# Kernel optimization log

Measured on AMD Instinct MI355X. Metric: run time of the kernel, lower is better.

Reference implementation:

```python
import jax, jax.numpy as jnp
import numpy as np

K = 3        # deform conv kernel size
STRIDE = 1
PAD = 1
DIL = 1


def setup_inputs() -> dict:
    key = jax.random.key(0)
    k1, k2, k3, k4 = jax.random.split(key, 4)
    B, C, H, W, O = 4, 256, 96, 96, 256
    x = jax.random.normal(k1, (B, C, H, W), jnp.float32)
    # offset-predicting conv: 3x3, stride 1, pad 1 -> 2*K*K channels
    # (source inits these to zero; use small random weights so offsets are
    # nonzero but sub-pixel scale, exercising the bilinear-sampling path)
    w_off = jax.random.normal(k2, (2 * K * K, C, 3, 3), jnp.float32) * 0.01
    b_off = jnp.zeros((2 * K * K,), jnp.float32)
    w_dc = jax.random.normal(k3, (O, C, K, K), jnp.float32) * (1.0 / np.sqrt(C * K * K))
    b_dc = jax.random.normal(k4, (O,), jnp.float32) * 0.01
    return {"x": x, "w_off": w_off, "b_off": b_off, "w_dc": w_dc, "b_dc": b_dc}


def _conv2d(x, w, b, stride, pad):
    out = jax.lax.conv_general_dilated(
        x, w, window_strides=(stride, stride),
        padding=[(pad, pad), (pad, pad)],
        dimension_numbers=("NCHW", "OIHW", "NCHW"))
    return out + b[None, :, None, None]


def _deform_conv(x, offset, w_dc, b_dc):
    # x: [B,C,H,W]; offset: [B, 2*K*K, Ho, Wo]; w_dc: [O,C,K,K]
    B, C, H, W = x.shape
    O = w_dc.shape[0]
    Ho = (H + 2 * PAD - DIL * (K - 1) - 1) // STRIDE + 1
    Wo = (W + 2 * PAD - DIL * (K - 1) - 1) // STRIDE + 1
    # mmcv layout: channel = (i*K + j)*2 + {0: dy, 1: dx}
    off = offset.reshape(B, K * K, 2, Ho, Wo)
    iy = jnp.repeat(jnp.arange(K), K)   # kernel row index per tap  [K*K]
    jx = jnp.tile(jnp.arange(K), K)     # kernel col index per tap  [K*K]
    base_y = (jnp.arange(Ho) * STRIDE - PAD)[None, :, None] + (iy * DIL)[:, None, None]  # [K2,Ho,1]
    base_x = (jnp.arange(Wo) * STRIDE - PAD)[None, None, :] + (jx * DIL)[:, None, None]  # [K2,1,Wo]
    py = base_y[None].astype(x.dtype) + off[:, :, 0]  # [B,K2,Ho,Wo]
    px = base_x[None].astype(x.dtype) + off[:, :, 1]  # [B,K2,Ho,Wo]

    y0 = jnp.floor(py)
    x0 = jnp.floor(px)
    ly = py - y0
    lx = px - x0
    y0i = y0.astype(jnp.int32)
    x0i = x0.astype(jnp.int32)

    flat = x.reshape(B, C, H * W)

    def corner(yi, xi, wgt):
        # zero-padding bilinear: out-of-range corners contribute 0
        valid = ((yi >= 0) & (yi < H) & (xi >= 0) & (xi < W)).astype(x.dtype)
        idx = jnp.clip(yi, 0, H - 1) * W + jnp.clip(xi, 0, W - 1)  # [B,K2,Ho,Wo]
        g = jnp.take_along_axis(flat, idx.reshape(B, 1, -1), axis=2)
        g = g.reshape(B, C, K * K, Ho, Wo)
        return g * (wgt * valid)[:, None]  # broadcast over channels

    val = (corner(y0i, x0i, (1 - ly) * (1 - lx))
           + corner(y0i, x0i + 1, (1 - ly) * lx)
           + corner(y0i + 1, x0i, ly * (1 - lx))
           + corner(y0i + 1, x0i + 1, ly * lx))  # [B,C,K2,Ho,Wo]

    out = jnp.einsum("bckhw,ock->bohw", val, w_dc.reshape(O, C, K * K))
    return out + b_dc[None, :, None, None]


def reference(x, w_off, b_off, w_dc, b_dc):
    offset = _conv2d(x, w_off, b_off, stride=1, pad=1)  # [B, 2*K*K, H, W]
    return _deform_conv(x, offset, w_dc, b_dc)
```

## Files before the change

kernel.cpp:

```cpp
#include <hip/hip_runtime.h>
#include <hip/hip_fp16.h>
#include <math.h>

#define BB   4
#define CC   256
#define HH   96
#define WW   96
#define OO   256
#define HW   9216
#define KDIM 2304
#define OFFC 18
#define NKC  36


typedef short bf16x8 __attribute__((ext_vector_type(8)));
typedef float f32x4  __attribute__((ext_vector_type(4)));
typedef unsigned int u32x4 __attribute__((ext_vector_type(4)));

#define WS_V_SZ    (36864ull * 4608ull)
#define WS_WB_OFF  WS_V_SZ
#define WS_WB_SZ   (256ull * 4608ull)
#define WS_META_OFF (WS_WB_OFF + WS_WB_SZ)
#define WS_META_SZ (4ull * 9ull * 9216ull * 16ull)
#define WS_WOFF_OFF (WS_META_OFF + 0x200000ull)
#define WS_NEED    (WS_META_OFF + WS_META_SZ)

__device__ __forceinline__ unsigned short f2bfu(float f) {
    unsigned u = __float_as_uint(f);
    unsigned r = (u + 0x7fffu + ((u >> 16) & 1u)) >> 16;
    return (unsigned short)r;
}
__device__ __forceinline__ unsigned pack2(float lo, float hi) {
    return (unsigned)f2bfu(lo) | ((unsigned)f2bfu(hi) << 16);
}
__device__ __forceinline__ void gload16(const void* g, void* l) {
    __builtin_amdgcn_global_load_lds((const __attribute__((address_space(1))) void*)g,
                                     (__attribute__((address_space(3))) void*)l, 16, 0, 0);
}

__device__ __forceinline__ uint4 make_meta(int pr, int t, float dy, float dx) {
    int oh = pr / WW, ow = pr - oh * WW;
    float py = (float)(oh - 1 + t / 3) + dy;
    float px = (float)(ow - 1 + (t % 3)) + dx;
    float y0f = floorf(py), x0f = floorf(px);
    int y0 = (int)y0f, x0 = (int)x0f;
    float ly = py - y0f, lx = px - x0f;
    float wy0 = (y0 >= 0 && y0 < HH) ? 1.f - ly : 0.f;
    float wy1 = (y0 + 1 >= 0 && y0 + 1 < HH) ? ly : 0.f;
    float u0 = (x0 >= 0 && x0 < WW) ? 1.f - lx : 0.f;
    float u1 = (x0 + 1 >= 0 && x0 + 1 < WW) ? lx : 0.f;
    int pb = min(max(x0, 0), WW - 2);
    float s0, s1;
    if (x0 < 0)           { s0 = u1; s1 = 0.f; }
    else if (x0 > WW - 2) { s0 = 0.f; s1 = u0; }
    else                  { s0 = u0; s1 = u1; }
    int cy0 = min(max(y0, 0), HH - 1);
    int cy1 = min(max(y0 + 1, 0), HH - 1);
    uint4 m;
    m.x = (unsigned)(cy0 * WW + pb);
    m.y = (unsigned)(cy1 * WW + pb);
    m.z = pack2(wy0 * s0, wy0 * s1);
    m.w = pack2(wy1 * s0, wy1 * s1);
    return m;
}


__global__ __launch_bounds__(256)
void woff_kernel(const float* __restrict__ w_off, char* __restrict__ Woff_b)
{
    int kc  = blockIdx.x;
    int tid = threadIdx.x;
    int so  = tid >> 3, sq = tid & 7;
    int tap = kc >> 2, cb = (kc & 3) * 64;
    uint4 pk; pk.x = pk.y = pk.z = pk.w = 0u;
    if (so < OFFC) {
        const float* wr = w_off + (size_t)so * KDIM + (size_t)(cb + sq * 8) * 9 + tap;
        float wv[8];
        #pragma unroll
        for (int i = 0; i < 8; ++i) wv[i] = wr[i * 9];
        pk.x = pack2(wv[0], wv[1]); pk.y = pack2(wv[2], wv[3]);
        pk.z = pack2(wv[4], wv[5]); pk.w = pack2(wv[6], wv[7]);
    }
    *(uint4*)(Woff_b + (size_t)kc * 4096 + so * 128 + ((sq * 16) ^ ((so & 7) << 4))) = pk;
}

__global__ __launch_bounds__(512)
void offset_meta_kernel2(const float* __restrict__ x,
                         const char* __restrict__ Woff_b,
                         const float* __restrict__ b_off,
                         unsigned* __restrict__ meta2_ws)
{
    __shared__ __align__(16) char Asw[64 * 128];
    __shared__ __align__(16) char Wl[32 * 128];
    __shared__ float Dsh[64][21];

    const int tid = threadIdx.x;
    const int fin = ((blockIdx.x & 7) * 72) + (blockIdx.x >> 3);
    const int b   = fin / 144;
    const int pr0 = (fin % 144) * 64;
    const float* xb = x + (size_t)b * CC * HW;

    const int w    = tid >> 6;
    const int l15  = tid & 15;
    const int l4   = (tid >> 4) & 3;
    const int pf   = w & 3;
    const int of   = w >> 2;
    const int sp   = tid & 63;
    const int kq   = tid >> 6;

    const int prg = pr0 + sp;
    const int oh = prg / WW, ow = prg - (prg / WW) * WW;

    f32x4 acc = (f32x4){0.f, 0.f, 0.f, 0.f};

    for (int kc = 0; kc < NKC; ++kc) {
        const int tap = kc >> 2;
        const int cb  = (kc & 3) * 64;
        if (w < 4)
            gload16(Woff_b + (size_t)kc * 4096 + (size_t)tid * 16, Wl + w * 1024);
        {
            int iy = oh + tap / 3 - 1;
            int ix = ow + tap % 3 - 1;
            bool ok = (iy >= 0) & (iy < HH) & (ix >= 0) & (ix < WW);
            const float* xp = xb + (size_t)(cb + kq * 8) * HW + iy * WW + ix;
            float v[8];
            #pragma unroll
            for (int e = 0; e < 8; ++e)
                v[e] = ok ? xp[(size_t)e * HW] : 0.f;
            uint4 pk;
            pk.x = pack2(v[0], v[1]); pk.y = pack2(v[2], v[3]);
            pk.z = pack2(v[4], v[5]); pk.w = pack2(v[6], v[7]);
            *(uint4*)(Asw + sp * 128 + ((kq * 16) ^ ((sp & 7) << 4))) = pk;
        }
        __syncthreads();
        {
            int p_loc = pf * 16 + l15;
            unsigned aswz = (unsigned)((p_loc & 7) << 4);
            int o_loc = of * 16 + l15;
            unsigned oswz = (unsigned)((o_loc & 7) << 4);
            #pragma unroll
            for (int ks = 0; ks < 2; ++ks) {
                bf16x8 a  = *(const bf16x8*)(Asw + p_loc * 128 + ((ks * 64 + l4 * 16) ^ aswz));
                bf16x8 bw = *(const bf16x8*)(Wl + o_loc * 128 + ((ks * 64 + l4 * 16) ^ oswz));
                acc = __builtin_amdgcn_mfma_f32_16x16x32_bf16(a, bw, acc, 0, 0, 0);
            }
        }
        __syncthreads();
    }

    {
        int o = of * 16 + l15;
        if (o < OFFC) {
            float bo = b_off[o];
            #pragma unroll
            for (int r = 0; r < 4; ++r)
                Dsh[pf * 16 + l4 * 4 + r][o] = acc[r] + bo;
        }
    }
    __syncthreads();
    for (int s = tid; s < 9 * 64; s += 512) {
        int t = s >> 6, pl = s & 63;
        int pr = pr0 + pl;
        float dy = Dsh[pl][2 * t];
        float dx = Dsh[pl][2 * t + 1];
        unsigned lo = (unsigned)__half_as_ushort(__float2half(dy));
        unsigned hi = (unsigned)__half_as_ushort(__float2half(dx));
        meta2_ws[((size_t)b * 9 + t) * HW + pr] = lo | (hi << 16);
    }
}

__global__ __launch_bounds__(256)
void wconv_kernel(const float* __restrict__ w_dc, char* __restrict__ wb)
{
    int idx = blockIdx.x * 256 + (int)threadIdx.x;
    int o   = idx / 288;
    int rem = idx - o * 288;
    int ch  = rem >> 3;
    int q   = rem & 7;
    int tap = ch >> 2;
    int c0  = (ch & 3) * 64 + q * 8;
    const float* wr = w_dc + (size_t)o * KDIM + (size_t)c0 * 9 + tap;
    float wv[8];
    #pragma unroll
    for (int i = 0; i < 8; ++i) wv[i] = wr[i * 9];
    uint4 pk;
    pk.x = pack2(wv[0], wv[1]); pk.y = pack2(wv[2], wv[3]);
    pk.z = pack2(wv[4], wv[5]); pk.w = pack2(wv[6], wv[7]);
    *(uint4*)(wb + (size_t)o * 4608 + ch * 128 + ((q * 16) ^ ((o & 7) << 4))) = pk;
}

#define GT_P   576
#define GT_WIN 14
__global__ __launch_bounds__(512, 4)
void gather_kernel9(const float* __restrict__ x,
                    const unsigned* __restrict__ meta2,
                    char* __restrict__ Vg)
{
    __shared__ __align__(16) unsigned short Xs[GT_WIN * 2 * 100 * 8];
    __shared__ unsigned Md[9 * GT_P];

    int bid  = blockIdx.x;
    int fin  = (bid & 7) * 128 + (bid >> 3);
    int tile = fin >> 4;
    int cq   = fin & 15;
    int b    = tile >> 4;
    int h0   = (tile & 15) * 6;
    int c0   = cq * 16;
    int tid  = threadIdx.x;
    int prow0 = tile * GT_P;

    int r0 = h0 - 3; r0 = r0 < 0 ? 0 : (r0 > 82 ? 82 : r0);

    for (int s = tid; s < 9 * GT_P; s += 512) {
        int t = s / GT_P, pl = s - t * GT_P;
        Md[s] = meta2[((size_t)b * 9 + t) * HW + h0 * WW + pl];
    }

    const float* xb = x + ((size_t)b * CC + c0) * HW + r0 * WW;
    for (int s = tid; s < GT_WIN * 2 * 96; s += 512) {
        int col = s % 96;
        int rem = s / 96;
        int chh = rem & 1;
        int row = rem >> 1;
        const float* g = xb + (size_t)(chh * 8) * HW + row * WW + col;
        uint4 pk;
        pk.x = pack2(g[0],              g[(size_t)1 * HW]);
        pk.y = pack2(g[(size_t)2 * HW], g[(size_t)3 * HW]);
        pk.z = pack2(g[(size_t)4 * HW], g[(size_t)5 * HW]);
        pk.w = pack2(g[(size_t)6 * HW], g[(size_t)7 * HW]);
        *(uint4*)&Xs[(((row * 2 + chh) * 100) + col) * 8] = pk;
    }
    __syncthreads();

    const int chh  = tid & 1;
    const int lsub = (tid & 63) >> 1;
    const int w    = tid >> 6;
    const float* xg = x + ((size_t)b * CC + c0 + chh * 8) * HW;
    const int chunk_hi = (cq >> 2) * 128;
    const int base_in_chunk = (cq & 3) * 32 + chh * 16;

    for (int pass = 0; pass < 3; ++pass) {
        int i = pass * 256 + w * 32 + lsub;
        if (i >= GT_P) break;
        int oh = h0 + i / WW, ow = i - (i / WW) * WW;
        char* vrow0 = Vg + (size_t)(prow0 + i) * 4608;
        const int inchunk = base_in_chunk ^ ((i & 7) << 4);
        #pragma unroll
        for (int t = 0; t < 9; ++t) {
            unsigned md = Md[t * GT_P + i];
            float dy = __half2float(__ushort_as_half((unsigned short)(md & 0xffffu)));
            float dx = __half2float(__ushort_as_half((unsigned short)(md >> 16)));
            float py = (float)(oh - 1 + t / 3) + dy;
            float px = (float)(ow - 1 + t % 3) + dx;
            float y0f = floorf(py), x0f = floorf(px);
            int y0 = (int)y0f, x0 = (int)x0f;
            float ly = py - y0f, lx = px - x0f;
            float wy0 = (y0 >= 0 && y0 < HH) ? 1.f - ly : 0.f;
            float wy1 = (y0 + 1 >= 0 && y0 + 1 < HH) ? ly : 0.f;
            float u0 = (x0 >= 0 && x0 < WW) ? 1.f - lx : 0.f;
            float u1 = (x0 + 1 >= 0 && x0 + 1 < WW) ? lx : 0.f;
            int pb = min(max(x0, 0), WW - 2);
            float s0, s1;
            if (x0 < 0)           { s0 = u1; s1 = 0.f; }
            else if (x0 > WW - 2) { s0 = 0.f; s1 = u0; }
            else                  { s0 = u0; s1 = u1; }
            int cy0 = min(max(y0, 0), HH - 1);
            int cy1 = min(max(y0 + 1, 0), HH - 1);
            float wa0 = wy0 * s0, wa1 = wy0 * s1;
            float wb0 = wy1 * s0, wb1 = wy1 * s1;
            float v[8];
            if (cy0 >= r0 && cy1 <= r0 + GT_WIN - 1) {
                int ra = ((cy0 - r0) * 2 + chh) * 100;
                int rb = ((cy1 - r0) * 2 + chh) * 100;
                u32x4 a0 = *(const u32x4*)&Xs[(ra + pb) * 8];
                u32x4 a1 = *(const u32x4*)&Xs[(ra + pb + 1) * 8];
                u32x4 b0 = *(const u32x4*)&Xs[(rb + pb) * 8];
                u32x4 b1 = *(const u32x4*)&Xs[(rb + pb + 1) * 8];
                #pragma unroll
                for (int k = 0; k < 8; ++k) {
                    unsigned sa0 = a0[k >> 1], sa1 = a1[k >> 1];
                    unsigned sb0 = b0[k >> 1], sb1 = b1[k >> 1];
                    float A0 = __uint_as_float((k & 1) ? (sa0 & 0xffff0000u) : (sa0 << 16));
                    float A1 = __uint_as_float((k & 1) ? (sa1 & 0xffff0000u) : (sa1 << 16));
                    float B0 = __uint_as_float((k & 1) ? (sb0 & 0xffff0000u) : (sb0 << 16));
                    float B1 = __uint_as_float((k & 1) ? (sb1 & 0xffff0000u) : (sb1 << 16));
                    v[k] = fmaf(wa0, A0, fmaf(wa1, A1, fmaf(wb0, B0, wb1 * B1)));
                }
            } else {
                const float* pa = xg + cy0 * WW + pb;
                const float* pq = xg + cy1 * WW + pb;
                #pragma unroll
                for (int k = 0; k < 8; ++k) {
                    float A0 = pa[(size_t)k * HW], A1 = pa[(size_t)k * HW + 1];
                    float B0 = pq[(size_t)k * HW], B1 = pq[(size_t)k * HW + 1];
                    v[k] = fmaf(wa0, A0, fmaf(wa1, A1, fmaf(wb0, B0, wb1 * B1)));
                }
            }
            u32x4 pk;
            pk.x = pack2(v[0], v[1]); pk.y = pack2(v[2], v[3]);
            pk.z = pack2(v[4], v[5]); pk.w = pack2(v[6], v[7]);
            *(u32x4*)(vrow0 + t * 512 + chunk_hi + inchunk) = pk;
        }
    }
}

__global__ __launch_bounds__(512)
void gemm_kernel(const char* __restrict__ Vg, const char* __restrict__ Wb,
                 const float* __restrict__ b_dc, float* __restrict__ out)
{
    __shared__ __align__(16) char Ab[2][128 * 128];
    __shared__ __align__(16) char Bb[2][128 * 128];

    int bid = blockIdx.x;
    int swzb = (bid & 7) * 72 + (bid >> 3);
    int pt = swzb >> 1, ot = swzb & 1;
    int tid = threadIdx.x;
    int wav = tid >> 6;
    const int l15 = tid & 15, l4 = (tid >> 4) & 3;
    const int wp = wav >> 2, wo = wav & 3;

    const char* Ag = Vg + (size_t)(pt * 128) * 4608;
    const char* Bg = Wb + (size_t)(ot * 128) * 4608;

    f32x4 acc[4][2];
    #pragma unroll
    for (int f = 0; f < 4; ++f)
        #pragma unroll
        for (int g = 0; g < 2; ++g)
            acc[f][g] = (f32x4){0.f, 0.f, 0.f, 0.f};

#define STAGE(bufi, t) {                                                         \
        const char* ag = Ag + (size_t)(t) * 128;                                 \
        const char* bg = Bg + (size_t)(t) * 128;                                 \
        _Pragma("unroll")                                                        \
        for (int i = 0; i < 2; ++i) {                                            \
            int u = i * 512 + tid;                                               \
            int row = u >> 3, cu = (u & 7) * 16;                                 \
            gload16(ag + (size_t)row * 4608 + cu,                                \
                    &Ab[bufi][(i * 512 + wav * 64) * 16]);                       \
            gload16(bg + (size_t)row * 4608 + cu,                                \
                    &Bb[bufi][(i * 512 + wav * 64) * 16]);                       \
        } }

    STAGE(0, 0);
    STAGE(1, 1);

    for (int t = 0; t < NKC; ++t) {
        int cb = t & 1;
        if (t < NKC - 1) {
            asm volatile("s_waitcnt vmcnt(4)" ::: "memory");
        } else {
            asm volatile("s_waitcnt vmcnt(0)" ::: "memory");
        }
        __builtin_amdgcn_s_barrier();
        asm volatile("" ::: "memory");
        __builtin_amdgcn_s_setprio(1);
        #pragma unroll
        for (int ks = 0; ks < 2; ++ks) {
            bf16x8 a[4], bw[2];
            #pragma unroll
            for (int f = 0; f < 4; ++f) {
                int p_loc = wp * 64 + f * 16 + l15;
                a[f] = *(const bf16x8*)(Ab[cb] + p_loc * 128 +
                                        ((ks * 64 + l4 * 16) ^ ((p_loc & 7) << 4)));
            }
            #pragma unroll
            for (int g = 0; g < 2; ++g) {
                int o_loc = wo * 32 + g * 16 + l15;
                bw[g] = *(const bf16x8*)(Bb[cb] + o_loc * 128 +
                                         ((ks * 64 + l4 * 16) ^ ((o_loc & 7) << 4)));
            }
            #pragma unroll
            for (int f = 0; f < 4; ++f)
                #pragma unroll
                for (int g = 0; g < 2; ++g)
                    acc[f][g] = __builtin_amdgcn_mfma_f32_16x16x32_bf16(a[f], bw[g], acc[f][g], 0, 0, 0);
        }
        __builtin_amdgcn_s_setprio(0);
        asm volatile("s_waitcnt lgkmcnt(0)" ::: "memory");
        __builtin_amdgcn_s_barrier();
        asm volatile("" ::: "memory");
        if (t + 2 < NKC) STAGE(cb, t + 2);
    }
#undef STAGE

    int b = pt / 72;
    int posr = (pt - b * 72) * 128;
    #pragma unroll
    for (int g = 0; g < 2; ++g) {
        int og = ot * 128 + wo * 32 + g * 16 + l15;
        float bias = b_dc[og];
        float* op = out + ((size_t)b * OO + og) * HW + posr + wp * 64 + l4 * 4;
        #pragma unroll
        for (int f = 0; f < 4; ++f) {
            f32x4 r = acc[f][g];
            float4 st;
            st.x = r[0] + bias; st.y = r[1] + bias;
            st.z = r[2] + bias; st.w = r[3] + bias;
            *(float4*)(op + f * 16) = st;
        }
    }
}


__global__ __launch_bounds__(256)
void offset_conv6_kernel(const float* __restrict__ x,
                         const float* __restrict__ w_off,
                         const float* __restrict__ b_off,
                         float* __restrict__ off)
{
    int bid   = blockIdx.x;
    int g     = bid % 3;
    int chunk = (bid / 3) % 36;
    int b     = bid / 108;
    int ocb   = g * 6;
    int pr    = chunk * 256 + (int)threadIdx.x;
    int oh    = pr / WW, ow = pr % WW;
    const float* xb = x + (size_t)b * CC * HW;

    float acc[6];
    #pragma unroll
    for (int i = 0; i < 6; ++i) acc[i] = b_off[ocb + i];

    bool interior = (oh >= 1) & (oh < HH - 1) & (ow >= 1) & (ow < WW - 1);
    if (interior) {
        const float* xp = xb + (oh - 1) * WW + (ow - 1);
        float xv[9];
        #pragma unroll
        for (int t = 0; t < 9; ++t) xv[t] = xp[(t / 3) * WW + (t % 3)];
        for (int c = 0; c < CC; ++c) {
            float xn[9];
            if (c + 1 < CC) {
                const float* xq = xp + (size_t)(c + 1) * HW;
                #pragma unroll
                for (int t = 0; t < 9; ++t) xn[t] = xq[(t / 3) * WW + (t % 3)];
            }
            #pragma unroll
            for (int i = 0; i < 6; ++i) {
                const float* wr = w_off + ((size_t)(ocb + i) * CC + c) * 9;
                #pragma unroll
                for (int t = 0; t < 9; ++t)
                    acc[i] = fmaf(xv[t], wr[t], acc[i]);
            }
            #pragma unroll
            for (int t = 0; t < 9; ++t) xv[t] = xn[t];
        }
    } else {
        for (int c = 0; c < CC; ++c) {
            const float* xc = xb + (size_t)c * HW;
            float xv[9];
            #pragma unroll
            for (int t = 0; t < 9; ++t) {
                int yy = oh + t / 3 - 1, xx = ow + t % 3 - 1;
                xv[t] = (yy >= 0 && yy < HH && xx >= 0 && xx < WW) ? xc[yy * WW + xx] : 0.f;
            }
            #pragma unroll
            for (int i = 0; i < 6; ++i) {
                const float* wr = w_off + ((size_t)(ocb + i) * CC + c) * 9;
                #pragma unroll
                for (int t = 0; t < 9; ++t)
                    acc[i] = fmaf(xv[t], wr[t], acc[i]);
            }
        }
    }
    #pragma unroll
    for (int i = 0; i < 6; ++i)
        off[((size_t)b * OFFC + ocb + i) * HW + pr] = acc[i];
}

__global__ __launch_bounds__(256)
void deform_mfma_kernel(const float* __restrict__ x,
                        const float* __restrict__ off,
                        const float* __restrict__ w_dc,
                        const float* __restrict__ b_dc,
                        float* __restrict__ out)
{
    __shared__ __align__(16) char VlB[128 * 128];
    __shared__ __align__(16) char WlB[128 * 128];
    __shared__ uint4 meta[9][128];

    const int tid  = threadIdx.x;
    const int ot   = blockIdx.x / 288;
    const int pt   = blockIdx.x % 288;
    const int pos0 = pt * 128;
    const int b    = pos0 / HW;
    const int posr = pos0 - b * HW;

    const float* offp = off + (size_t)b * OFFC * HW;
    for (int s = tid; s < 9 * 128; s += 256) {
        int tt = s >> 7, j = s & 127;
        int pr = posr + j;
        float dy = offp[(2 * tt) * HW + pr];
        float dx = offp[(2 * tt + 1) * HW + pr];
        meta[tt][j] = make_meta(pr, tt, dy, dx);
    }
    __syncthreads();

    const int l15 = tid & 15;
    const int l4  = (tid >> 4) & 3;
    const int wav = tid >> 6;
    const int wp  = wav >> 1, wwo = wav & 1;
    const int j     = tid & 127;
    const int khalf = tid >> 7;
    const int wo_o  = tid >> 4;
    const int wk    = (tid & 15) * 4;

    const float* wbase = w_dc + (size_t)(ot * 128) * KDIM;

    f32x4 acc[4][4];
    #pragma unroll
    for (int f = 0; f < 4; ++f)
        #pragma unroll
        for (int g = 0; g < 4; ++g)
            acc[f][g] = (f32x4){0.f, 0.f, 0.f, 0.f};

    for (int k0 = 0; k0 < KDIM; k0 += 64) {
        #pragma unroll
        for (int r = 0; r < 8; ++r) {
            int o = r * 16 + wo_o;
            const float4 wv = *(const float4*)(wbase + (size_t)o * KDIM + k0 + wk);
            uint2 u;
            u.x = pack2(wv.x, wv.y);
            u.y = pack2(wv.z, wv.w);
            *(uint2*)(WlB + o * 128 + ((wk * 2) ^ ((o & 7) << 4))) = u;
        }
        {
            unsigned kb = (unsigned)(k0 + khalf * 32);
            unsigned c  = kb / 9u;
            unsigned tt = kb - c * 9u;
            const float* xc = x + (size_t)((unsigned)b * CC + c) * HW;
            char* vrow = VlB + j * 128;
            const unsigned swz = (unsigned)((j & 7) << 4);
            #pragma unroll
            for (int g = 0; g < 4; ++g) {
                float v[8];
                #pragma unroll
                for (int e = 0; e < 8; ++e) {
                    uint4 m = meta[tt][j];
                    float A0 = xc[m.x], A1 = xc[m.x + 1];
                    float B0 = xc[m.y], B1 = xc[m.y + 1];
                    float a0 = __uint_as_float(m.z << 16);
                    float a1 = __uint_as_float(m.z & 0xffff0000u);
                    float b0 = __uint_as_float(m.w << 16);
                    float b1 = __uint_as_float(m.w & 0xffff0000u);
                    v[e] = fmaf(a0, A0, fmaf(a1, A1, fmaf(b0, B0, b1 * B1)));
                    ++tt;
                    if (tt == 9u) { tt = 0u; xc += HW; }
                }
                uint4 pk;
                pk.x = pack2(v[0], v[1]); pk.y = pack2(v[2], v[3]);
                pk.z = pack2(v[4], v[5]); pk.w = pack2(v[6], v[7]);
                *(uint4*)(vrow + (((unsigned)(khalf * 64 + g * 16)) ^ swz)) = pk;
            }
        }
        __syncthreads();

        #pragma unroll
        for (int ks = 0; ks < 2; ++ks) {
            bf16x8 a[4], bw[4];
            #pragma unroll
            for (int f = 0; f < 4; ++f) {
                int p_loc = wp * 64 + f * 16 + l15;
                a[f] = *(const bf16x8*)(VlB + p_loc * 128 +
                                        ((ks * 64 + l4 * 16) ^ ((p_loc & 7) << 4)));
            }
            #pragma unroll
            for (int g = 0; g < 4; ++g) {
                int o_loc = wwo * 64 + g * 16 + l15;
                bw[g] = *(const bf16x8*)(WlB + o_loc * 128 +
                                         ((ks * 64 + l4 * 16) ^ ((o_loc & 7) << 4)));
            }
            #pragma unroll
            for (int f = 0; f < 4; ++f)
                #pragma unroll
                for (int g = 0; g < 4; ++g)
                    acc[f][g] = __builtin_amdgcn_mfma_f32_16x16x32_bf16(a[f], bw[g], acc[f][g], 0, 0, 0);
        }
        __syncthreads();
    }

    #pragma unroll
    for (int g = 0; g < 4; ++g) {
        int og = ot * 128 + wwo * 64 + g * 16 + l15;
        float bias = b_dc[og];
        float* op = out + ((size_t)b * OO + og) * HW + posr + wp * 64 + l4 * 4;
        #pragma unroll
        for (int f = 0; f < 4; ++f) {
            f32x4 r = acc[f][g];
            float4 st;
            st.x = r[0] + bias; st.y = r[1] + bias;
            st.z = r[2] + bias; st.w = r[3] + bias;
            *(float4*)(op + f * 16) = st;
        }
    }
}

extern "C" void kernel_launch(void* const* d_in, const int* in_sizes, int n_in,
                              void* d_out, int out_size, void* d_ws, size_t ws_size,
                              hipStream_t stream)
{
    const float* x     = (const float*)d_in[0];
    const float* w_off = (const float*)d_in[1];
    const float* b_off = (const float*)d_in[2];
    const float* w_dc  = (const float*)d_in[3];
    const float* b_dc  = (const float*)d_in[4];
    float* out = (float*)d_out;

    if (ws_size >= WS_NEED) {
        char*     ws    = (char*)d_ws;
        char*     Vg    = ws;
        char*     Wb    = ws + WS_WB_OFF;
        unsigned* meta2 = (unsigned*)(ws + WS_META_OFF);
        char*     Woffb = ws + WS_WOFF_OFF;
        woff_kernel<<<NKC, 256, 0, stream>>>(w_off, Woffb);
        wconv_kernel<<<288, 256, 0, stream>>>(w_dc, Wb);
        offset_meta_kernel2<<<576, 512, 0, stream>>>(x, Woffb, b_off, meta2);
        gather_kernel9<<<1024, 512, 0, stream>>>(x, meta2, Vg);
        gemm_kernel<<<576, 512, 0, stream>>>(Vg, Wb, b_dc, out);
    } else {
        float* off = (float*)d_ws;
        offset_conv6_kernel<<<BB * 36 * 3, 256, 0, stream>>>(x, w_off, b_off, off);
        deform_mfma_kernel<<<(OO / 128) * (BB * HW / 128), 256, 0, stream>>>(x, off, w_dc, b_dc, out);
    }
}
```

Before: 181.4 us.

## Split offset conv K across waves with smaller tiles; drop gather LDS metadata staging

The offset-conv kernel now processes 32 pixels per block instead of 64, doubling the grid to 1152 blocks. Its eight waves are split into two K-halves whose partial MFMA results are summed through shared memory together with the bias. The gather kernel no longer stages the offset metadata in LDS and reads it directly from global memory per tap. Its occupancy hint is raised from 4 to 6 blocks per CU. The aim is more parallelism in the small offset GEMM and less LDS use in the gather kernel, at the cost of extra reduction work and uncoalesced metadata loads.

```diff
diff --git a/kernel.cpp b/kernel.cpp
--- a/kernel.cpp
+++ b/kernel.cpp
@@ -85,28 +85,29 @@
 }
 
 __global__ __launch_bounds__(512)
-void offset_meta_kernel2(const float* __restrict__ x,
+void offset_meta_kernel3(const float* __restrict__ x,
                          const char* __restrict__ Woff_b,
                          const float* __restrict__ b_off,
                          unsigned* __restrict__ meta2_ws)
 {
-    __shared__ __align__(16) char Asw[64 * 128];
+    __shared__ __align__(16) char Asw[32 * 128];
     __shared__ __align__(16) char Wl[32 * 128];
-    __shared__ float Dsh[64][21];
+    __shared__ float Dsh[2][32][21];
 
     const int tid = threadIdx.x;
-    const int fin = ((blockIdx.x & 7) * 72) + (blockIdx.x >> 3);
-    const int b   = fin / 144;
-    const int pr0 = (fin % 144) * 64;
+    const int fin = ((blockIdx.x & 7) * 144) + (blockIdx.x >> 3);
+    const int b   = fin / 288;
+    const int pr0 = (fin % 288) * 32;
     const float* xb = x + (size_t)b * CC * HW;
 
     const int w    = tid >> 6;
     const int l15  = tid & 15;
     const int l4   = (tid >> 4) & 3;
-    const int pf   = w & 3;
-    const int of   = w >> 2;
-    const int sp   = tid & 63;
-    const int kq   = tid >> 6;
+    const int pf   = w & 1;
+    const int of   = (w >> 1) & 1;
+    const int ksw  = w >> 2;
+    const int sp   = tid & 31;
+    const int kq   = tid >> 5;
 
     const int prg = pr0 + sp;
     const int oh = prg / WW, ow = prg - (prg / WW) * WW;
@@ -116,34 +117,30 @@
     for (int kc = 0; kc < NKC; ++kc) {
         const int tap = kc >> 2;
         const int cb  = (kc & 3) * 64;
-        if (w < 4)
-            gload16(Woff_b + (size_t)kc * 4096 + (size_t)tid * 16, Wl + w * 1024);
+        if (tid < 256)
+            gload16(Woff_b + (size_t)kc * 4096 + (size_t)tid * 16, Wl + (tid >> 6) * 1024);
         {
             int iy = oh + tap / 3 - 1;
             int ix = ow + tap % 3 - 1;
             bool ok = (iy >= 0) & (iy < HH) & (ix >= 0) & (ix < WW);
-            const float* xp = xb + (size_t)(cb + kq * 8) * HW + iy * WW + ix;
-            float v[8];
-            #pragma unroll
-            for (int e = 0; e < 8; ++e)
+            const float* xp = xb + (size_t)(cb + kq * 4) * HW + iy * WW + ix;
+            float v[4];
+            #pragma unroll
+            for (int e = 0; e < 4; ++e)
                 v[e] = ok ? xp[(size_t)e * HW] : 0.f;
-            uint4 pk;
+            uint2 pk;
             pk.x = pack2(v[0], v[1]); pk.y = pack2(v[2], v[3]);
-            pk.z = pack2(v[4], v[5]); pk.w = pack2(v[6], v[7]);
-            *(uint4*)(Asw + sp * 128 + ((kq * 16) ^ ((sp & 7) << 4))) = pk;
+            *(uint2*)(Asw + sp * 128 + ((kq * 8) ^ ((sp & 7) << 4))) = pk;
         }
         __syncthreads();
         {
             int p_loc = pf * 16 + l15;
-            unsigned aswz = (unsigned)((p_loc & 7) << 4);
             int o_loc = of * 16 + l15;
-            unsigned oswz = (unsigned)((o_loc & 7) << 4);
-            #pragma unroll
-            for (int ks = 0; ks < 2; ++ks) {
-                bf16x8 a  = *(const bf16x8*)(Asw + p_loc * 128 + ((ks * 64 + l4 * 16) ^ aswz));
-                bf16x8 bw = *(const bf16x8*)(Wl + o_loc * 128 + ((ks * 64 + l4 * 16) ^ oswz));
-                acc = __builtin_amdgcn_mfma_f32_16x16x32_bf16(a, bw, acc, 0, 0, 0);
-            }
+            bf16x8 a  = *(const bf16x8*)(Asw + p_loc * 128 +
+                                         ((ksw * 64 + l4 * 16) ^ ((p_loc & 7) << 4)));
+            bf16x8 bw = *(const bf16x8*)(Wl + o_loc * 128 +
+                                         ((ksw * 64 + l4 * 16) ^ ((o_loc & 7) << 4)));
+            acc = __builtin_amdgcn_mfma_f32_16x16x32_bf16(a, bw, acc, 0, 0, 0);
         }
         __syncthreads();
     }
@@ -151,18 +148,17 @@
     {
         int o = of * 16 + l15;
         if (o < OFFC) {
-            float bo = b_off[o];
             #pragma unroll
             for (int r = 0; r < 4; ++r)
-                Dsh[pf * 16 + l4 * 4 + r][o] = acc[r] + bo;
+                Dsh[ksw][pf * 16 + l4 * 4 + r][o] = acc[r];
         }
     }
     __syncthreads();
-    for (int s = tid; s < 9 * 64; s += 512) {
-        int t = s >> 6, pl = s & 63;
+    for (int s = tid; s < 9 * 32; s += 512) {
+        int t = s >> 5, pl = s & 31;
         int pr = pr0 + pl;
-        float dy = Dsh[pl][2 * t];
-        float dx = Dsh[pl][2 * t + 1];
+        float dy = Dsh[0][pl][2 * t]     + Dsh[1][pl][2 * t]     + b_off[2 * t];
+        float dx = Dsh[0][pl][2 * t + 1] + Dsh[1][pl][2 * t + 1] + b_off[2 * t + 1];
         unsigned lo = (unsigned)__half_as_ushort(__float2half(dy));
         unsigned hi = (unsigned)__half_as_ushort(__float2half(dx));
         meta2_ws[((size_t)b * 9 + t) * HW + pr] = lo | (hi << 16);
@@ -191,13 +187,12 @@
 
 #define GT_P   576
 #define GT_WIN 14
-__global__ __launch_bounds__(512, 4)
-void gather_kernel9(const float* __restrict__ x,
-                    const unsigned* __restrict__ meta2,
-                    char* __restrict__ Vg)
+__global__ __launch_bounds__(512, 6)
+void gather_kernel10(const float* __restrict__ x,
+                     const unsigned* __restrict__ meta2,
+                     char* __restrict__ Vg)
 {
     __shared__ __align__(16) unsigned short Xs[GT_WIN * 2 * 100 * 8];
-    __shared__ unsigned Md[9 * GT_P];
 
     int bid  = blockIdx.x;
     int fin  = (bid & 7) * 128 + (bid >> 3);
@@ -210,11 +205,6 @@
     int prow0 = tile * GT_P;
 
     int r0 = h0 - 3; r0 = r0 < 0 ? 0 : (r0 > 82 ? 82 : r0);
-
-    for (int s = tid; s < 9 * GT_P; s += 512) {
-        int t = s / GT_P, pl = s - t * GT_P;
-        Md[s] = meta2[((size_t)b * 9 + t) * HW + h0 * WW + pl];
-    }
 
     const float* xb = x + ((size_t)b * CC + c0) * HW + r0 * WW;
     for (int s = tid; s < GT_WIN * 2 * 96; s += 512) {
@@ -238,6 +228,7 @@
     const float* xg = x + ((size_t)b * CC + c0 + chh * 8) * HW;
     const int chunk_hi = (cq >> 2) * 128;
     const int base_in_chunk = (cq & 3) * 32 + chh * 16;
+    const size_t mbase = (size_t)b * 9 * HW + (size_t)h0 * WW;
 
     for (int pass = 0; pass < 3; ++pass) {
         int i = pass * 256 + w * 32 + lsub;
@@ -247,7 +238,7 @@
         const int inchunk = base_in_chunk ^ ((i & 7) << 4);
         #pragma unroll
         for (int t = 0; t < 9; ++t) {
-            unsigned md = Md[t * GT_P + i];
+            unsigned md = meta2[mbase + (size_t)t * HW + i];
             float dy = __half2float(__ushort_as_half((unsigned short)(md & 0xffffu)));
             float dx = __half2float(__ushort_as_half((unsigned short)(md >> 16)));
             float py = (float)(oh - 1 + t / 3) + dy;
@@ -614,8 +605,8 @@
         char*     Woffb = ws + WS_WOFF_OFF;
         woff_kernel<<<NKC, 256, 0, stream>>>(w_off, Woffb);
         wconv_kernel<<<288, 256, 0, stream>>>(w_dc, Wb);
-        offset_meta_kernel2<<<576, 512, 0, stream>>>(x, Woffb, b_off, meta2);
-        gather_kernel9<<<1024, 512, 0, stream>>>(x, meta2, Vg);
+        offset_meta_kernel3<<<1152, 512, 0, stream>>>(x, Woffb, b_off, meta2);
+        gather_kernel10<<<1024, 512, 0, stream>>>(x, meta2, Vg);
         gemm_kernel<<<576, 512, 0, stream>>>(Vg, Wb, b_dc, out);
     } else {
         float* off = (float*)d_ws;
```

After: 181.9 us. About the same (+0.3%).
